# Kernel tuning notes

Hardware: AMD Instinct MI355X
Metric: run time of the kernel (lower is better)

The kernel has to match this reference:

```python
import jax, jax.numpy as jnp
import numpy as np

NH = 16
D = 1024
B, T = 4, 4096


def setup_inputs() -> dict:
    key = jax.random.key(0)
    k1, k2, k3, k4 = jax.random.split(key, 4)
    x = jax.random.normal(k1, (B, T, D), dtype=jnp.float32)
    phi = jax.random.normal(k2, (B, T), dtype=jnp.float32)
    W_attn = jax.random.normal(k3, (D, D), dtype=jnp.float32) * 0.02
    W_proj = jax.random.normal(k4, (D, D), dtype=jnp.float32) * 0.02
    gamma = jnp.ones((NH, 1), dtype=jnp.float32)
    temp = jnp.ones((NH, 1), dtype=jnp.float32)
    return {"x": x, "phi": phi, "W_attn": W_attn, "W_proj": W_proj,
            "gamma": gamma, "temp": temp}


def reference(x, phi, W_attn, W_proj, gamma, temp):
    Bb, Tt, d = x.shape
    hd = d // NH
    # c_attn (no bias), split heads: [B, nh, T, hd]
    w = (x @ W_attn.T).reshape(Bb, Tt, NH, hd).transpose(0, 2, 1, 3)
    w_sq = w * w
    denom = jnp.maximum(jnp.cumsum(w_sq, axis=-2), 1e-12)
    w_norm = w_sq / denom
    tssa_score = w_norm.sum(-1) * temp                       # [B, nh, T]
    phi_Q = phi[:, None, :]                                  # [B, 1, T]
    steps = jnp.arange(1, Tt + 1, dtype=x.dtype)
    mean_phi = jnp.cumsum(phi, axis=-1)[:, None, :] / steps  # running mean of phi
    penalty = (phi_Q - mean_phi) ** 2                        # [B, 1, T]
    score = tssa_score - gamma * penalty                     # [B, nh, T]
    alpha = jax.nn.softmax(score, axis=1)                    # softmax over HEADS (dim=1)
    dots = jnp.cumsum(w_sq * alpha[..., None], axis=-2) / (
        jnp.cumsum(alpha, axis=-1)[..., None] + 1e-8)
    attn = jnp.minimum(1.0 / (1.0 + dots), 10000.0)
    y = -w * alpha[..., None] * attn                          # [B, nh, T, hd]
    y = y.transpose(0, 2, 1, 3).reshape(Bb, Tt, d)
    y = y @ W_proj.T                                          # dropout is identity (p=0 / eval)
    return (y, alpha)
```

## Files before the change

### kernel.cpp

```cpp
#include <hip/hip_runtime.h>
#include <hip/hip_bf16.h>
#include <stdint.h>

#define NHh 16
#define Dm  1024
#define HD  64
#define Bb  4
#define Tt  4096
#define NCH 128
#define CHL 32

#define BM 256
#define BN 256
#define BK 64
#define NKT (Dm / BK)

using bf16 = __hip_bfloat16;
typedef __attribute__((ext_vector_type(8))) short short8;
typedef __attribute__((ext_vector_type(4))) float f32x4;

__device__ __forceinline__ float bf2f(bf16 v) { return __bfloat162float(v); }

__device__ __forceinline__ float b2f(unsigned short u) {
  union { unsigned int i; float f; } x; x.i = ((unsigned int)u) << 16; return x.f;
}

__device__ __forceinline__ float frcp(float x) {
  float r; asm("v_rcp_f32 %0, %1" : "=v"(r) : "v"(x)); return r;
}

__device__ __forceinline__ void gld_lds16(const void* g, void* l) {
  __builtin_amdgcn_global_load_lds(
      (const __attribute__((address_space(1))) unsigned int*)g,
      (__attribute__((address_space(3))) unsigned int*)l, 16, 0, 0);
}

template <bool OUT_BF16, bool WRITE_S1>
__global__ __launch_bounds__(512, 2) void gemm256(const bf16* __restrict__ A,
                                                  const bf16* __restrict__ W,
                                                  void* __restrict__ Cout,
                                                  float* __restrict__ S1,
                                                  int M, int N, int K) {
  extern __shared__ char smem[];
  const int tid  = threadIdx.x;
  const int lane = tid & 63;
  const int wave = tid >> 6;
  const int bid = blockIdx.x;
  const int swz = (bid & 7) * 32 + (bid >> 3);
  const int bn = (swz & 3) * BN;
  const int bm = (swz >> 2) * BM;
  const int wm = (wave >> 1) * 64;
  const int wn = (wave & 1) * 128;
  const int quad = lane >> 4;
  const int l16  = lane & 15;

  const int srow = wave * 8 + (lane >> 3);
  const int scol = (((lane & 7) ^ (lane >> 3)) << 3);

  const bf16* Abase = A + (size_t)(bm + srow) * K + scol;
  const bf16* Wbase = W + (size_t)(bn + srow) * K + scol;

  f32x4 acc[4][8] = {};

#define SLAB_A(buf, n) (smem + (buf) * 65536 + (n) * 8192 + wave * 1024)
#define SLAB_B(buf, n) (smem + (buf) * 65536 + 32768 + (n) * 8192 + wave * 1024)
#define STAGE_A(buf, n, k0) gld_lds16(Abase + (size_t)(n) * 64 * K + (k0), SLAB_A(buf, n))
#define STAGE_B(buf, n, k0) gld_lds16(Wbase + (size_t)(n) * 64 * K + (k0), SLAB_B(buf, n))
#define LD_FRAG(base, r, s) (*(const short8*)((base) + (size_t)(r) * 128 + ((((s) ^ ((r) & 7))) << 4)))

  STAGE_A(0, 0, 0); STAGE_A(0, 1, 0); STAGE_A(0, 2, 0); STAGE_A(0, 3, 0);
  STAGE_B(0, 0, 0); STAGE_B(0, 1, 0); STAGE_B(0, 2, 0); STAGE_B(0, 3, 0);
  asm volatile("s_waitcnt vmcnt(0)" ::: "memory");
  __builtin_amdgcn_s_barrier();
  __builtin_amdgcn_sched_barrier(0);

  short8 af[4][2], bfv[4][2];
  for (int t = 0; t < NKT; t++) {
    const int buf = t & 1;
    const char* aL = smem + buf * 65536;
    const char* bL = aL + 32768;
    const int k0n = (t + 1) * BK;
    const bool pf = (t + 1 < NKT);

    if (pf) {
      STAGE_A(buf ^ 1, 0, k0n); STAGE_A(buf ^ 1, 1, k0n);
      STAGE_A(buf ^ 1, 2, k0n); STAGE_A(buf ^ 1, 3, k0n);
      STAGE_B(buf ^ 1, 0, k0n); STAGE_B(buf ^ 1, 2, k0n);
    }
#pragma unroll
    for (int mi = 0; mi < 4; mi++) {
      const int r = wm + mi * 16 + l16;
      af[mi][0] = LD_FRAG(aL, r, quad);
      af[mi][1] = LD_FRAG(aL, r, quad + 4);
    }
#pragma unroll
    for (int nj = 0; nj < 4; nj++) {
      const int r = wn + nj * 16 + l16;
      bfv[nj][0] = LD_FRAG(bL, r, quad);
      bfv[nj][1] = LD_FRAG(bL, r, quad + 4);
    }
    __builtin_amdgcn_s_setprio(1);
#pragma unroll
    for (int mi = 0; mi < 4; mi++)
#pragma unroll
      for (int nj = 0; nj < 4; nj++) {
        acc[mi][nj] = __builtin_amdgcn_mfma_f32_16x16x32_bf16(af[mi][0], bfv[nj][0], acc[mi][nj], 0, 0, 0);
        acc[mi][nj] = __builtin_amdgcn_mfma_f32_16x16x32_bf16(af[mi][1], bfv[nj][1], acc[mi][nj], 0, 0, 0);
      }
    __builtin_amdgcn_s_setprio(0);
    if (pf) { asm volatile("s_waitcnt vmcnt(6)" ::: "memory"); }
    else    { asm volatile("s_waitcnt vmcnt(0)" ::: "memory"); }
    __builtin_amdgcn_s_barrier();
    __builtin_amdgcn_sched_barrier(0);

    if (pf) { STAGE_B(buf ^ 1, 1, k0n); STAGE_B(buf ^ 1, 3, k0n); }
#pragma unroll
    for (int nj = 0; nj < 4; nj++) {
      const int r = wn + 64 + nj * 16 + l16;
      bfv[nj][0] = LD_FRAG(bL, r, quad);
      bfv[nj][1] = LD_FRAG(bL, r, quad + 4);
    }
    __builtin_amdgcn_s_setprio(1);
#pragma unroll
    for (int mi = 0; mi < 4; mi++)
#pragma unroll
      for (int nj = 0; nj < 4; nj++) {
        acc[mi][nj + 4] = __builtin_amdgcn_mfma_f32_16x16x32_bf16(af[mi][0], bfv[nj][0], acc[mi][nj + 4], 0, 0, 0);
        acc[mi][nj + 4] = __builtin_amdgcn_mfma_f32_16x16x32_bf16(af[mi][1], bfv[nj][1], acc[mi][nj + 4], 0, 0, 0);
      }
    __builtin_amdgcn_s_setprio(0);
    asm volatile("s_waitcnt vmcnt(2)" ::: "memory");
    __builtin_amdgcn_s_barrier();
    __builtin_amdgcn_sched_barrier(0);
  }

#pragma unroll
  for (int nj = 0; nj < 8; nj++) {
    const int col = bn + wn + nj * 16 + l16;
    if constexpr (OUT_BF16) {
      float ss0 = 0.f, ss1 = 0.f;
#pragma unroll
      for (int mi = 0; mi < 4; mi++) {
        float csum = 0.f;
#pragma unroll
        for (int r = 0; r < 4; r++) {
          const int row = bm + wm + mi * 16 + quad * 4 + r;
          const bf16 hv = __float2bfloat16(acc[mi][nj][r]);
          ((bf16*)Cout)[(size_t)row * N + col] = hv;
          if constexpr (WRITE_S1) { const float fv = bf2f(hv); csum += fv * fv; }
        }
        if constexpr (WRITE_S1) { if (mi < 2) ss0 += csum; else ss1 += csum; }
      }
      if constexpr (WRITE_S1) {
        ss0 += __shfl_xor(ss0, 16, 64); ss0 += __shfl_xor(ss0, 32, 64);
        ss1 += __shfl_xor(ss1, 16, 64); ss1 += __shfl_xor(ss1, 32, 64);
        if (quad == 0) {
          const int h = col >> 6, d = col & 63;
          const int r0 = bm + wm;
          const int b  = r0 >> 12;
          const int c0 = (r0 & (Tt - 1)) >> 5;
          float* s1p = S1 + (((size_t)(b * NHh + h) * NCH) + c0) * HD + d;
          s1p[0]  = ss0;
          s1p[HD] = ss1;
        }
      }
    } else {
#pragma unroll
      for (int mi = 0; mi < 4; mi++)
#pragma unroll
        for (int r = 0; r < 4; r++) {
          const int row = bm + wm + mi * 16 + quad * 4 + r;
          ((float*)Cout)[(size_t)row * N + col] = acc[mi][nj][r];
        }
    }
  }
#undef SLAB_A
#undef SLAB_B
#undef STAGE_A
#undef STAGE_B
#undef LD_FRAG
}

__global__ __launch_bounds__(256) void prep(const float* __restrict__ x,
                                            const float* __restrict__ Wa,
                                            const float* __restrict__ Wp,
                                            const float* __restrict__ phi,
                                            bf16* __restrict__ x_bf,
                                            bf16* __restrict__ Wa_bf,
                                            bf16* __restrict__ Wp_bf,
                                            float* __restrict__ penalty) {
  const int bid = blockIdx.x;
  if (bid < 1536) {
    const float* in;
    bf16* out;
    int n, nblk, b0;
    if (bid < 1024)      { in = x;  out = x_bf;  n = Bb * Tt * Dm; nblk = 1024; b0 = 0; }
    else if (bid < 1280) { in = Wa; out = Wa_bf; n = Dm * Dm;      nblk = 256;  b0 = 1024; }
    else                 { in = Wp; out = Wp_bf; n = Dm * Dm;      nblk = 256;  b0 = 1280; }
    const int stride = nblk * 256;
    for (int i = (bid - b0) * 256 + threadIdx.x; i * 4 < n; i += stride) {
      const float4 v = *(const float4*)(in + (size_t)i * 4);
      ushort4 o;
      o.x = __bfloat16_as_ushort(__float2bfloat16(v.x));
      o.y = __bfloat16_as_ushort(__float2bfloat16(v.y));
      o.z = __bfloat16_as_ushort(__float2bfloat16(v.z));
      o.w = __bfloat16_as_ushort(__float2bfloat16(v.w));
      *(ushort4*)(out + (size_t)i * 4) = o;
    }
  } else {
    const int b = bid - 1536;
    const int tid = threadIdx.x;
    const int lane = tid & 63, wid = tid >> 6;
    __shared__ float wsum[4];
    __shared__ float carry_s;
    if (tid == 0) carry_s = 0.f;
    __syncthreads();
    for (int r = 0; r < Tt / 256; r++) {
      const int t = r * 256 + tid;
      const float v = phi[b * Tt + t];
      float incl = v;
#pragma unroll
      for (int off = 1; off < 64; off <<= 1) {
        float nn = __shfl_up(incl, off, 64);
        if (lane >= off) incl += nn;
      }
      if (lane == 63) wsum[wid] = incl;
      __syncthreads();
      float woff = carry_s;
      for (int wpre = 0; wpre < wid; wpre++) woff += wsum[wpre];
      const float csum = woff + incl;
      const float mean = csum / (float)(t + 1);
      const float dphi = v - mean;
      penalty[b * Tt + t] = dphi * dphi;
      __syncthreads();
      if (tid == 0) carry_s += wsum[0] + wsum[1] + wsum[2] + wsum[3];
      __syncthreads();
    }
  }
}

__global__ __launch_bounds__(256) void mid_fused(const bf16* __restrict__ w,
                                                 const float* __restrict__ S1,
                                                 const float* __restrict__ temp,
                                                 const float* __restrict__ gamma,
                                                 const float* __restrict__ penalty,
                                                 float* __restrict__ alpha_f,
                                                 float* __restrict__ S2,
                                                 float* __restrict__ SA) {
  const int c = blockIdx.x, b = blockIdx.y;
  const int tid = threadIdx.x, h = tid >> 4, l = tid & 15;
  __shared__ float sm_t[CHL][NHh + 1];
  __shared__ float sm_a[CHL][NHh + 1];
  __shared__ float sm_g[NHh], sm_tv[NHh];
  if (tid < NHh) { sm_g[tid] = gamma[tid]; sm_tv[tid] = temp[tid]; }

  const float4* p4 = (const float4*)(S1 + (((size_t)(b * NHh + h) * NCH)) * HD + l * 4);
  float4 s0 = {0,0,0,0}, s1v = {0,0,0,0}, s2v = {0,0,0,0}, s3v = {0,0,0,0};
  int cc = 0;
  for (; cc + 4 <= c; cc += 4) {
    const float4 v0 = p4[(size_t)cc * 16];
    const float4 v1 = p4[(size_t)(cc + 1) * 16];
    const float4 v2 = p4[(size_t)(cc + 2) * 16];
    const float4 v3 = p4[(size_t)(cc + 3) * 16];
    s0.x += v0.x; s0.y += v0.y; s0.z += v0.z; s0.w += v0.w;
    s1v.x += v1.x; s1v.y += v1.y; s1v.z += v1.z; s1v.w += v1.w;
    s2v.x += v2.x; s2v.y += v2.y; s2v.z += v2.z; s2v.w += v2.w;
    s3v.x += v3.x; s3v.y += v3.y; s3v.z += v3.z; s3v.w += v3.w;
  }
  for (; cc < c; cc++) {
    const float4 v0 = p4[(size_t)cc * 16];
    s0.x += v0.x; s0.y += v0.y; s0.z += v0.z; s0.w += v0.w;
  }
  float a0 = s0.x + s1v.x + s2v.x + s3v.x;
  float a1 = s0.y + s1v.y + s2v.y + s3v.y;
  float a2 = s0.z + s1v.z + s2v.z + s3v.z;
  float a3 = s0.w + s1v.w + s2v.w + s3v.w;
  __syncthreads();

  const bf16* wp = w + ((size_t)(b * Tt + c * CHL)) * Dm + h * HD + l * 4;
  const float tv = sm_tv[h];
#pragma unroll 8
  for (int i = 0; i < CHL; i++) {
    const ushort4 v = *(const ushort4*)(wp + (size_t)i * Dm);
    const float f0 = b2f(v.x), f1 = b2f(v.y), f2 = b2f(v.z), f3 = b2f(v.w);
    const float q0 = f0 * f0, q1 = f1 * f1, q2 = f2 * f2, q3 = f3 * f3;
    a0 += q0; a1 += q1; a2 += q2; a3 += q3;
    float val = q0 * frcp(fmaxf(a0, 1e-12f)) + q1 * frcp(fmaxf(a1, 1e-12f))
              + q2 * frcp(fmaxf(a2, 1e-12f)) + q3 * frcp(fmaxf(a3, 1e-12f));
    val += __shfl_xor(val, 1, 64);
    val += __shfl_xor(val, 2, 64);
    val += __shfl_xor(val, 4, 64);
    val += __shfl_xor(val, 8, 64);
    if (l == 0) sm_t[i][h] = tv * val;
  }
  __syncthreads();

  if (tid < CHL) {
    const int t = tid;
    const float pen = penalty[(size_t)b * Tt + c * CHL + t];
    float sc[NHh];
    float mx = -1e30f;
#pragma unroll
    for (int hh = 0; hh < NHh; hh++) {
      sc[hh] = sm_t[t][hh] - sm_g[hh] * pen;
      mx = fmaxf(mx, sc[hh]);
    }
    float sum = 0.f;
#pragma unroll
    for (int hh = 0; hh < NHh; hh++) { const float e = __expf(sc[hh] - mx); sc[hh] = e; sum += e; }
    const float inv = 1.f / sum;
#pragma unroll
    for (int hh = 0; hh < NHh; hh++) sm_a[t][hh] = sc[hh] * inv;
  }
  __syncthreads();

#pragma unroll
  for (int k2 = 0; k2 < CHL / 16; k2++) {
    const int t = k2 * 16 + l;
    alpha_f[((size_t)(b * NHh + h)) * Tt + c * CHL + t] = sm_a[t][h];
  }

  float d0 = 0.f, d1 = 0.f, d2 = 0.f, d3 = 0.f, sa = 0.f;
#pragma unroll 8
  for (int i = 0; i < CHL; i++) {
    const float a = sm_a[i][h];
    const ushort4 v = *(const ushort4*)(wp + (size_t)i * Dm);
    const float f0 = b2f(v.x), f1 = b2f(v.y), f2 = b2f(v.z), f3 = b2f(v.w);
    d0 += f0 * f0 * a; d1 += f1 * f1 * a; d2 += f2 * f2 * a; d3 += f3 * f3 * a;
    sa += a;
  }
  float4 o; o.x = d0; o.y = d1; o.z = d2; o.w = d3;
  *(float4*)&S2[(((size_t)(b * NHh + h) * NCH) + c) * HD + l * 4] = o;
  if (l == 0) SA[(size_t)(b * NHh + h) * NCH + c] = sa;
}

__global__ __launch_bounds__(256) void y_phase3(const bf16* __restrict__ w,
                                                const float* __restrict__ alpha_f,
                                                const float* __restrict__ S2,
                                                const float* __restrict__ SA,
                                                bf16* __restrict__ yprime) {
  const int c = blockIdx.x, b = blockIdx.y;
  const int tid = threadIdx.x, h = tid >> 4, l = tid & 15;

  const float* sap = SA + (size_t)(b * NHh + h) * NCH;
  float sa_part = 0.f;
  for (int cc = l; cc < c; cc += 16) sa_part += sap[cc];
  sa_part += __shfl_xor(sa_part, 1, 64);
  sa_part += __shfl_xor(sa_part, 2, 64);
  sa_part += __shfl_xor(sa_part, 4, 64);
  sa_part += __shfl_xor(sa_part, 8, 64);
  float acca = sa_part;

  const float4* p4 = (const float4*)(S2 + (((size_t)(b * NHh + h) * NCH)) * HD + l * 4);
  float4 s0 = {0,0,0,0}, s1v = {0,0,0,0}, s2v = {0,0,0,0}, s3v = {0,0,0,0};
  int cc = 0;
  for (; cc + 4 <= c; cc += 4) {
    const float4 v0 = p4[(size_t)cc * 16];
    const float4 v1 = p4[(size_t)(cc + 1) * 16];
    const float4 v2 = p4[(size_t)(cc + 2) * 16];
    const float4 v3 = p4[(size_t)(cc + 3) * 16];
    s0.x += v0.x; s0.y += v0.y; s0.z += v0.z; s0.w += v0.w;
    s1v.x += v1.x; s1v.y += v1.y; s1v.z += v1.z; s1v.w += v1.w;
    s2v.x += v2.x; s2v.y += v2.y; s2v.z += v2.z; s2v.w += v2.w;
    s3v.x += v3.x; s3v.y += v3.y; s3v.z += v3.z; s3v.w += v3.w;
  }
  for (; cc < c; cc++) {
    const float4 v0 = p4[(size_t)cc * 16];
    s0.x += v0.x; s0.y += v0.y; s0.z += v0.z; s0.w += v0.w;
  }
  float a0 = s0.x + s1v.x + s2v.x + s3v.x;
  float a1 = s0.y + s1v.y + s2v.y + s3v.y;
  float a2 = s0.z + s1v.z + s2v.z + s3v.z;
  float a3 = s0.w + s1v.w + s2v.w + s3v.w;

  const bf16* wp = w + ((size_t)(b * Tt + c * CHL)) * Dm + h * HD + l * 4;
  const float* ap = alpha_f + (size_t)(b * NHh + h) * Tt + c * CHL;
  bf16* yp = yprime + ((size_t)(b * Tt + c * CHL)) * Dm + h * HD + l * 4;
#pragma unroll 8
  for (int i = 0; i < CHL; i++) {
    const float a = ap[i];
    const ushort4 v = *(const ushort4*)(wp + (size_t)i * Dm);
    const float f0 = b2f(v.x), f1 = b2f(v.y), f2 = b2f(v.z), f3 = b2f(v.w);
    a0 += f0 * f0 * a; a1 += f1 * f1 * a; a2 += f2 * f2 * a; a3 += f3 * f3 * a;
    acca += a;
    const float rinv = frcp(acca + 1e-8f);
    const float at0 = fminf(frcp(1.f + a0 * rinv), 10000.f);
    const float at1 = fminf(frcp(1.f + a1 * rinv), 10000.f);
    const float at2 = fminf(frcp(1.f + a2 * rinv), 10000.f);
    const float at3 = fminf(frcp(1.f + a3 * rinv), 10000.f);
    ushort4 o;
    o.x = __bfloat16_as_ushort(__float2bfloat16(-f0 * a * at0));
    o.y = __bfloat16_as_ushort(__float2bfloat16(-f1 * a * at1));
    o.z = __bfloat16_as_ushort(__float2bfloat16(-f2 * a * at2));
    o.w = __bfloat16_as_ushort(__float2bfloat16(-f3 * a * at3));
    *(ushort4*)(yp + (size_t)i * Dm) = o;
  }
}

extern "C" void kernel_launch(void* const* d_in, const int* in_sizes, int n_in,
                              void* d_out, int out_size, void* d_ws, size_t ws_size,
                              hipStream_t stream) {
  const float* x     = (const float*)d_in[0];
  const float* phi   = (const float*)d_in[1];
  const float* Wattn = (const float*)d_in[2];
  const float* Wproj = (const float*)d_in[3];
  const float* gamma = (const float*)d_in[4];
  const float* temp  = (const float*)d_in[5];

  float* y_out    = (float*)d_out;
  float* alpha_f  = y_out + (size_t)Bb * Tt * Dm;

  char* ws = (char*)d_ws;
  bf16*  x_bf   = (bf16*)ws;  ws += (size_t)Bb * Tt * Dm * 2;
  bf16*  Wa_bf  = (bf16*)ws;  ws += (size_t)Dm * Dm * 2;
  bf16*  Wp_bf  = (bf16*)ws;  ws += (size_t)Dm * Dm * 2;
  bf16*  w_bf   = (bf16*)ws;  ws += (size_t)Bb * Tt * Dm * 2;
  float* pen    = (float*)ws; ws += (size_t)Bb * Tt * 4;
  float* S1     = (float*)ws; ws += (size_t)Bb * NHh * NCH * HD * 4;
  float* S2     = (float*)ws; ws += (size_t)Bb * NHh * NCH * HD * 4;
  float* SA     = (float*)ws; ws += (size_t)Bb * NHh * NCH * 4;
  bf16*  yprime = x_bf;

  static int attr_done = 0;
  if (!attr_done) {
    hipFuncSetAttribute((const void*)gemm256<true, true>,
                        hipFuncAttributeMaxDynamicSharedMemorySize, 131072);
    hipFuncSetAttribute((const void*)gemm256<false, false>,
                        hipFuncAttributeMaxDynamicSharedMemorySize, 131072);
    attr_done = 1;
  }

  const int M = Bb * Tt, N = Dm, K = Dm;
  dim3 gg((M / BM) * (N / BN)), gb(512);

  prep<<<dim3(1540), dim3(256), 0, stream>>>(x, Wattn, Wproj, phi, x_bf, Wa_bf, Wp_bf, pen);
  gemm256<true, true><<<gg, gb, 131072, stream>>>(x_bf, Wa_bf, (void*)w_bf, S1, M, N, K);
  mid_fused<<<dim3(NCH, Bb), dim3(256), 0, stream>>>(w_bf, S1, temp, gamma, pen,
                                                     alpha_f, S2, SA);
  y_phase3<<<dim3(NCH, Bb), dim3(256), 0, stream>>>(w_bf, alpha_f, S2, SA, yprime);
  gemm256<false, false><<<gg, gb, 131072, stream>>>(yprime, Wp_bf, (void*)y_out, nullptr, M, N, K);
}
```

Measured before the change: 253.7 us.

## Fuse fp32-to-bf16 conversion of x into first GEMM and stage bf16 output via LDS

The first GEMM now reads x directly as fp32, converts it to bf16 in registers and writes the swizzled tile into LDS. This removes the separate prep pass that wrote and re-read a bf16 copy of x. The bf16 output tile is also staged through LDS so it can be written to global memory in coalesced 16-byte chunks instead of scattered 2-byte stores. In exchange the A loads become register-routed with more vmcnt bookkeeping, use more VGPRs and fetch twice the bytes per k-tile.

```diff
diff --git a/kernel.cpp b/kernel.cpp
--- a/kernel.cpp
+++ b/kernel.cpp
@@ -35,8 +35,21 @@
       (__attribute__((address_space(3))) unsigned int*)l, 16, 0, 0);
 }
 
-template <bool OUT_BF16, bool WRITE_S1>
-__global__ __launch_bounds__(512, 2) void gemm256(const bf16* __restrict__ A,
+__device__ __forceinline__ short8 pack8(const float4& a, const float4& b) {
+  short8 r;
+  r[0] = (short)__bfloat16_as_ushort(__float2bfloat16(a.x));
+  r[1] = (short)__bfloat16_as_ushort(__float2bfloat16(a.y));
+  r[2] = (short)__bfloat16_as_ushort(__float2bfloat16(a.z));
+  r[3] = (short)__bfloat16_as_ushort(__float2bfloat16(a.w));
+  r[4] = (short)__bfloat16_as_ushort(__float2bfloat16(b.x));
+  r[5] = (short)__bfloat16_as_ushort(__float2bfloat16(b.y));
+  r[6] = (short)__bfloat16_as_ushort(__float2bfloat16(b.z));
+  r[7] = (short)__bfloat16_as_ushort(__float2bfloat16(b.w));
+  return r;
+}
+
+template <bool A_FP32, bool OUT_BF16, bool WRITE_S1>
+__global__ __launch_bounds__(512, 2) void gemm256(const void* __restrict__ Ain,
                                                   const bf16* __restrict__ W,
                                                   void* __restrict__ Cout,
                                                   float* __restrict__ S1,
@@ -57,47 +70,66 @@
   const int srow = wave * 8 + (lane >> 3);
   const int scol = (((lane & 7) ^ (lane >> 3)) << 3);
 
-  const bf16* Abase = A + (size_t)(bm + srow) * K + scol;
-  const bf16* Wbase = W + (size_t)(bn + srow) * K + scol;
+  const bf16*  Abase  = A_FP32 ? nullptr : ((const bf16*)Ain + (size_t)(bm + srow) * K + scol);
+  const float* Afbase = A_FP32 ? ((const float*)Ain + (size_t)(bm + srow) * K + scol) : nullptr;
+  const bf16*  Wbase  = W + (size_t)(bn + srow) * K + scol;
 
   f32x4 acc[4][8] = {};
+  float4 aL[4][2];
 
 #define SLAB_A(buf, n) (smem + (buf) * 65536 + (n) * 8192 + wave * 1024)
 #define SLAB_B(buf, n) (smem + (buf) * 65536 + 32768 + (n) * 8192 + wave * 1024)
 #define STAGE_A(buf, n, k0) gld_lds16(Abase + (size_t)(n) * 64 * K + (k0), SLAB_A(buf, n))
 #define STAGE_B(buf, n, k0) gld_lds16(Wbase + (size_t)(n) * 64 * K + (k0), SLAB_B(buf, n))
+#define LOADA(n, k0) do {                                                    \
+    const float* p_ = Afbase + (size_t)(n) * 64 * K + (k0);                  \
+    aL[n][0] = *(const float4*)p_;                                           \
+    aL[n][1] = *(const float4*)(p_ + 4);                                     \
+  } while (0)
+#define WRITEA(buf, n) do {                                                  \
+    *(short8*)(SLAB_A(buf, n) + lane * 16) = pack8(aL[n][0], aL[n][1]);      \
+  } while (0)
 #define LD_FRAG(base, r, s) (*(const short8*)((base) + (size_t)(r) * 128 + ((((s) ^ ((r) & 7))) << 4)))
 
-  STAGE_A(0, 0, 0); STAGE_A(0, 1, 0); STAGE_A(0, 2, 0); STAGE_A(0, 3, 0);
-  STAGE_B(0, 0, 0); STAGE_B(0, 1, 0); STAGE_B(0, 2, 0); STAGE_B(0, 3, 0);
-  asm volatile("s_waitcnt vmcnt(0)" ::: "memory");
+  if constexpr (A_FP32) {
+    LOADA(0, 0); LOADA(1, 0); LOADA(2, 0); LOADA(3, 0);
+    STAGE_B(0, 0, 0); STAGE_B(0, 1, 0); STAGE_B(0, 2, 0); STAGE_B(0, 3, 0);
+    asm volatile("s_waitcnt vmcnt(4)" ::: "memory");
+    WRITEA(0, 0); WRITEA(0, 1); WRITEA(0, 2); WRITEA(0, 3);
+    asm volatile("s_waitcnt vmcnt(0) lgkmcnt(0)" ::: "memory");
+  } else {
+    STAGE_A(0, 0, 0); STAGE_A(0, 1, 0); STAGE_A(0, 2, 0); STAGE_A(0, 3, 0);
+    STAGE_B(0, 0, 0); STAGE_B(0, 1, 0); STAGE_B(0, 2, 0); STAGE_B(0, 3, 0);
+    asm volatile("s_waitcnt vmcnt(0)" ::: "memory");
+  }
   __builtin_amdgcn_s_barrier();
   __builtin_amdgcn_sched_barrier(0);
 
   short8 af[4][2], bfv[4][2];
   for (int t = 0; t < NKT; t++) {
     const int buf = t & 1;
-    const char* aL = smem + buf * 65536;
-    const char* bL = aL + 32768;
+    const char* aLd = smem + buf * 65536;
+    const char* bLd = aLd + 32768;
     const int k0n = (t + 1) * BK;
     const bool pf = (t + 1 < NKT);
 
     if (pf) {
-      STAGE_A(buf ^ 1, 0, k0n); STAGE_A(buf ^ 1, 1, k0n);
-      STAGE_A(buf ^ 1, 2, k0n); STAGE_A(buf ^ 1, 3, k0n);
+      if constexpr (A_FP32) { LOADA(0, k0n); LOADA(1, k0n); LOADA(2, k0n); LOADA(3, k0n); }
+      else { STAGE_A(buf ^ 1, 0, k0n); STAGE_A(buf ^ 1, 1, k0n);
+             STAGE_A(buf ^ 1, 2, k0n); STAGE_A(buf ^ 1, 3, k0n); }
       STAGE_B(buf ^ 1, 0, k0n); STAGE_B(buf ^ 1, 2, k0n);
     }
 #pragma unroll
     for (int mi = 0; mi < 4; mi++) {
       const int r = wm + mi * 16 + l16;
-      af[mi][0] = LD_FRAG(aL, r, quad);
-      af[mi][1] = LD_FRAG(aL, r, quad + 4);
+      af[mi][0] = LD_FRAG(aLd, r, quad);
+      af[mi][1] = LD_FRAG(aLd, r, quad + 4);
     }
 #pragma unroll
     for (int nj = 0; nj < 4; nj++) {
       const int r = wn + nj * 16 + l16;
-      bfv[nj][0] = LD_FRAG(bL, r, quad);
-      bfv[nj][1] = LD_FRAG(bL, r, quad + 4);
+      bfv[nj][0] = LD_FRAG(bLd, r, quad);
+      bfv[nj][1] = LD_FRAG(bLd, r, quad + 4);
     }
     __builtin_amdgcn_s_setprio(1);
 #pragma unroll
@@ -108,18 +140,26 @@
         acc[mi][nj] = __builtin_amdgcn_mfma_f32_16x16x32_bf16(af[mi][1], bfv[nj][1], acc[mi][nj], 0, 0, 0);
       }
     __builtin_amdgcn_s_setprio(0);
-    if (pf) { asm volatile("s_waitcnt vmcnt(6)" ::: "memory"); }
-    else    { asm volatile("s_waitcnt vmcnt(0)" ::: "memory"); }
+    if (pf) {
+      if constexpr (A_FP32) { asm volatile("s_waitcnt vmcnt(10)" ::: "memory"); }
+      else                  { asm volatile("s_waitcnt vmcnt(6)" ::: "memory"); }
+    } else { asm volatile("s_waitcnt vmcnt(0)" ::: "memory"); }
     __builtin_amdgcn_s_barrier();
     __builtin_amdgcn_sched_barrier(0);
 
-    if (pf) { STAGE_B(buf ^ 1, 1, k0n); STAGE_B(buf ^ 1, 3, k0n); }
+    if (pf) {
+      if constexpr (A_FP32) {
+        asm volatile("s_waitcnt vmcnt(2)" ::: "memory");
+        WRITEA(buf ^ 1, 0); WRITEA(buf ^ 1, 1); WRITEA(buf ^ 1, 2); WRITEA(buf ^ 1, 3);
+      }
+    }
 #pragma unroll
     for (int nj = 0; nj < 4; nj++) {
       const int r = wn + 64 + nj * 16 + l16;
-      bfv[nj][0] = LD_FRAG(bL, r, quad);
-      bfv[nj][1] = LD_FRAG(bL, r, quad + 4);
-    }
+      bfv[nj][0] = LD_FRAG(bLd, r, quad);
+      bfv[nj][1] = LD_FRAG(bLd, r, quad + 4);
+    }
+    if (pf) { STAGE_B(buf ^ 1, 1, k0n); STAGE_B(buf ^ 1, 3, k0n); }
     __builtin_amdgcn_s_setprio(1);
 #pragma unroll
     for (int mi = 0; mi < 4; mi++)
@@ -129,24 +169,27 @@
         acc[mi][nj + 4] = __builtin_amdgcn_mfma_f32_16x16x32_bf16(af[mi][1], bfv[nj][1], acc[mi][nj + 4], 0, 0, 0);
       }
     __builtin_amdgcn_s_setprio(0);
-    asm volatile("s_waitcnt vmcnt(2)" ::: "memory");
+    if (pf) { asm volatile("s_waitcnt vmcnt(2) lgkmcnt(0)" ::: "memory"); }
+    else    { asm volatile("s_waitcnt vmcnt(0) lgkmcnt(0)" ::: "memory"); }
     __builtin_amdgcn_s_barrier();
     __builtin_amdgcn_sched_barrier(0);
   }
 
-#pragma unroll
-  for (int nj = 0; nj < 8; nj++) {
-    const int col = bn + wn + nj * 16 + l16;
-    if constexpr (OUT_BF16) {
+  if constexpr (OUT_BF16) {
+    ushort* cst = (ushort*)smem;
+#pragma unroll
+    for (int nj = 0; nj < 8; nj++) {
+      const int gcol = bn + wn + nj * 16 + l16;
       float ss0 = 0.f, ss1 = 0.f;
 #pragma unroll
       for (int mi = 0; mi < 4; mi++) {
         float csum = 0.f;
 #pragma unroll
         for (int r = 0; r < 4; r++) {
-          const int row = bm + wm + mi * 16 + quad * 4 + r;
+          const int row = wm + mi * 16 + quad * 4 + r;
+          const int col = wn + nj * 16 + l16;
           const bf16 hv = __float2bfloat16(acc[mi][nj][r]);
-          ((bf16*)Cout)[(size_t)row * N + col] = hv;
+          cst[(row * 512 + ((col * 2) ^ ((row & 7) << 4))) >> 1] = __bfloat16_as_ushort(hv);
           if constexpr (WRITE_S1) { const float fv = bf2f(hv); csum += fv * fv; }
         }
         if constexpr (WRITE_S1) { if (mi < 2) ss0 += csum; else ss1 += csum; }
@@ -155,7 +198,7 @@
         ss0 += __shfl_xor(ss0, 16, 64); ss0 += __shfl_xor(ss0, 32, 64);
         ss1 += __shfl_xor(ss1, 16, 64); ss1 += __shfl_xor(ss1, 32, 64);
         if (quad == 0) {
-          const int h = col >> 6, d = col & 63;
+          const int h = gcol >> 6, d = gcol & 63;
           const int r0 = bm + wm;
           const int b  = r0 >> 12;
           const int c0 = (r0 & (Tt - 1)) >> 5;
@@ -164,7 +207,21 @@
           s1p[HD] = ss1;
         }
       }
-    } else {
+    }
+    asm volatile("s_waitcnt lgkmcnt(0)" ::: "memory");
+    __builtin_amdgcn_s_barrier();
+#pragma unroll
+    for (int it = 0; it < 16; it++) {
+      const int idx = it * 512 + tid;
+      const int row = idx >> 5;
+      const int ch  = idx & 31;
+      const short8 v = *(const short8*)(smem + row * 512 + ((ch ^ (row & 7)) << 4));
+      *(short8*)((bf16*)Cout + (size_t)(bm + row) * N + bn + ch * 8) = v;
+    }
+  } else {
+#pragma unroll
+    for (int nj = 0; nj < 8; nj++) {
+      const int col = bn + wn + nj * 16 + l16;
 #pragma unroll
       for (int mi = 0; mi < 4; mi++)
 #pragma unroll
@@ -178,26 +235,24 @@
 #undef SLAB_B
 #undef STAGE_A
 #undef STAGE_B
+#undef LOADA
+#undef WRITEA
 #undef LD_FRAG
 }
 
-__global__ __launch_bounds__(256) void prep(const float* __restrict__ x,
-                                            const float* __restrict__ Wa,
+__global__ __launch_bounds__(256) void prep(const float* __restrict__ Wa,
                                             const float* __restrict__ Wp,
                                             const float* __restrict__ phi,
-                                            bf16* __restrict__ x_bf,
                                             bf16* __restrict__ Wa_bf,
                                             bf16* __restrict__ Wp_bf,
                                             float* __restrict__ penalty) {
   const int bid = blockIdx.x;
-  if (bid < 1536) {
-    const float* in;
-    bf16* out;
-    int n, nblk, b0;
-    if (bid < 1024)      { in = x;  out = x_bf;  n = Bb * Tt * Dm; nblk = 1024; b0 = 0; }
-    else if (bid < 1280) { in = Wa; out = Wa_bf; n = Dm * Dm;      nblk = 256;  b0 = 1024; }
-    else                 { in = Wp; out = Wp_bf; n = Dm * Dm;      nblk = 256;  b0 = 1280; }
-    const int stride = nblk * 256;
+  if (bid < 512) {
+    const float* in = (bid < 256) ? Wa : Wp;
+    bf16* out = (bid < 256) ? Wa_bf : Wp_bf;
+    const int b0 = (bid < 256) ? 0 : 256;
+    const int n = Dm * Dm;
+    const int stride = 256 * 256;
     for (int i = (bid - b0) * 256 + threadIdx.x; i * 4 < n; i += stride) {
       const float4 v = *(const float4*)(in + (size_t)i * 4);
       ushort4 o;
@@ -208,7 +263,7 @@
       *(ushort4*)(out + (size_t)i * 4) = o;
     }
   } else {
-    const int b = bid - 1536;
+    const int b = bid - 512;
     const int tid = threadIdx.x;
     const int lane = tid & 63, wid = tid >> 6;
     __shared__ float wsum[4];
@@ -411,21 +466,20 @@
   float* alpha_f  = y_out + (size_t)Bb * Tt * Dm;
 
   char* ws = (char*)d_ws;
-  bf16*  x_bf   = (bf16*)ws;  ws += (size_t)Bb * Tt * Dm * 2;
   bf16*  Wa_bf  = (bf16*)ws;  ws += (size_t)Dm * Dm * 2;
   bf16*  Wp_bf  = (bf16*)ws;  ws += (size_t)Dm * Dm * 2;
   bf16*  w_bf   = (bf16*)ws;  ws += (size_t)Bb * Tt * Dm * 2;
+  bf16*  yprime = (bf16*)ws;  ws += (size_t)Bb * Tt * Dm * 2;
   float* pen    = (float*)ws; ws += (size_t)Bb * Tt * 4;
   float* S1     = (float*)ws; ws += (size_t)Bb * NHh * NCH * HD * 4;
   float* S2     = (float*)ws; ws += (size_t)Bb * NHh * NCH * HD * 4;
   float* SA     = (float*)ws; ws += (size_t)Bb * NHh * NCH * 4;
-  bf16*  yprime = x_bf;
 
   static int attr_done = 0;
   if (!attr_done) {
-    hipFuncSetAttribute((const void*)gemm256<true, true>,
+    hipFuncSetAttribute((const void*)gemm256<true, true, true>,
                         hipFuncAttributeMaxDynamicSharedMemorySize, 131072);
-    hipFuncSetAttribute((const void*)gemm256<false, false>,
+    hipFuncSetAttribute((const void*)gemm256<false, false, false>,
                         hipFuncAttributeMaxDynamicSharedMemorySize, 131072);
     attr_done = 1;
   }
@@ -433,10 +487,10 @@
   const int M = Bb * Tt, N = Dm, K = Dm;
   dim3 gg((M / BM) * (N / BN)), gb(512);
 
-  prep<<<dim3(1540), dim3(256), 0, stream>>>(x, Wattn, Wproj, phi, x_bf, Wa_bf, Wp_bf, pen);
-  gemm256<true, true><<<gg, gb, 131072, stream>>>(x_bf, Wa_bf, (void*)w_bf, S1, M, N, K);
+  prep<<<dim3(516), dim3(256), 0, stream>>>(Wattn, Wproj, phi, Wa_bf, Wp_bf, pen);
+  gemm256<true, true, true><<<gg, gb, 131072, stream>>>(x, Wa_bf, (void*)w_bf, S1, M, N, K);
   mid_fused<<<dim3(NCH, Bb), dim3(256), 0, stream>>>(w_bf, S1, temp, gamma, pen,
                                                      alpha_f, S2, SA);
   y_phase3<<<dim3(NCH, Bb), dim3(256), 0, stream>>>(w_bf, alpha_f, S2, SA, yprime);
-  gemm256<false, false><<<gg, gb, 131072, stream>>>(yprime, Wp_bf, (void*)y_out, nullptr, M, N, K);
-}
+  gemm256<false, false, false><<<gg, gb, 131072, stream>>>(yprime, Wp_bf, (void*)y_out, nullptr, M, N, K);
+}
```

Result: slower. 270.1 us (+6.5%).

## Shrink GEMM tiles to 256x128x32 with simpler double-buffered pipeline

Applied to the files above, without the earlier changes.

Changes the bf16 GEMM from 256x256x64 tiles to 256x128x32 tiles, which cuts LDS use per block from 128KB to 48KB and raises the launch-bounds occupancy hint from 2 to 4. The staggered B-slab prefetch with partial vmcnt waits is replaced by one full-wait barrier per k-step, and the block swizzle is adjusted for 8 column tiles. The aim is more blocks in flight and better CU coverage (512 blocks instead of 256), at the cost of less data reuse per tile, twice as many barriers and no overlap of loads inside a k-step.

```diff
diff --git a/kernel.cpp b/kernel.cpp
--- a/kernel.cpp
+++ b/kernel.cpp
@@ -11,8 +11,8 @@
 #define CHL 32
 
 #define BM 256
-#define BN 256
-#define BK 64
+#define BN 128
+#define BK 32
 #define NKT (Dm / BK)
 
 using bf16 = __hip_bfloat16;
@@ -36,7 +36,7 @@
 }
 
 template <bool OUT_BF16, bool WRITE_S1>
-__global__ __launch_bounds__(512, 2) void gemm256(const bf16* __restrict__ A,
+__global__ __launch_bounds__(512, 4) void gemm256(const bf16* __restrict__ A,
                                                   const bf16* __restrict__ W,
                                                   void* __restrict__ Cout,
                                                   float* __restrict__ S1,
@@ -46,96 +46,60 @@
   const int lane = tid & 63;
   const int wave = tid >> 6;
   const int bid = blockIdx.x;
-  const int swz = (bid & 7) * 32 + (bid >> 3);
-  const int bn = (swz & 3) * BN;
-  const int bm = (swz >> 2) * BM;
+  const int swz = (bid & 7) * 64 + (bid >> 3);
+  const int bn = (swz & 7) * BN;
+  const int bm = (swz >> 3) * BM;
   const int wm = (wave >> 1) * 64;
-  const int wn = (wave & 1) * 128;
+  const int wn = (wave & 1) * 64;
   const int quad = lane >> 4;
   const int l16  = lane & 15;
 
-  const int srow = wave * 8 + (lane >> 3);
-  const int scol = (((lane & 7) ^ (lane >> 3)) << 3);
+  const int srow = wave * 16 + (lane >> 2);
+  const int scol = (((lane & 3) ^ ((lane >> 3) & 3)) << 3);
 
   const bf16* Abase = A + (size_t)(bm + srow) * K + scol;
   const bf16* Wbase = W + (size_t)(bn + srow) * K + scol;
 
-  f32x4 acc[4][8] = {};
-
-#define SLAB_A(buf, n) (smem + (buf) * 65536 + (n) * 8192 + wave * 1024)
-#define SLAB_B(buf, n) (smem + (buf) * 65536 + 32768 + (n) * 8192 + wave * 1024)
-#define STAGE_A(buf, n, k0) gld_lds16(Abase + (size_t)(n) * 64 * K + (k0), SLAB_A(buf, n))
-#define STAGE_B(buf, n, k0) gld_lds16(Wbase + (size_t)(n) * 64 * K + (k0), SLAB_B(buf, n))
-#define LD_FRAG(base, r, s) (*(const short8*)((base) + (size_t)(r) * 128 + ((((s) ^ ((r) & 7))) << 4)))
-
-  STAGE_A(0, 0, 0); STAGE_A(0, 1, 0); STAGE_A(0, 2, 0); STAGE_A(0, 3, 0);
-  STAGE_B(0, 0, 0); STAGE_B(0, 1, 0); STAGE_B(0, 2, 0); STAGE_B(0, 3, 0);
+  f32x4 acc[4][4] = {};
+
+#define SLAB_A(buf, n) (smem + (buf) * 24576 + (n) * 8192 + wave * 1024)
+#define SLAB_B(buf)    (smem + (buf) * 24576 + 16384 + wave * 1024)
+#define STAGE_A(buf, n, k0) gld_lds16(Abase + (size_t)(n) * 128 * K + (k0), SLAB_A(buf, n))
+#define STAGE_B(buf, k0)    gld_lds16(Wbase + (k0), SLAB_B(buf))
+#define LD_FRAG(sb, r, c) (*(const short8*)((sb) + (size_t)(r) * 64 + ((((c) ^ (((r) >> 1) & 3))) << 4)))
+
+  STAGE_A(0, 0, 0); STAGE_A(0, 1, 0); STAGE_B(0, 0);
   asm volatile("s_waitcnt vmcnt(0)" ::: "memory");
   __builtin_amdgcn_s_barrier();
   __builtin_amdgcn_sched_barrier(0);
 
-  short8 af[4][2], bfv[4][2];
+  short8 af[4], bf8[4];
   for (int t = 0; t < NKT; t++) {
     const int buf = t & 1;
-    const char* aL = smem + buf * 65536;
-    const char* bL = aL + 32768;
+    const char* aL = smem + buf * 24576;
+    const char* bL = aL + 16384;
     const int k0n = (t + 1) * BK;
-    const bool pf = (t + 1 < NKT);
-
-    if (pf) {
-      STAGE_A(buf ^ 1, 0, k0n); STAGE_A(buf ^ 1, 1, k0n);
-      STAGE_A(buf ^ 1, 2, k0n); STAGE_A(buf ^ 1, 3, k0n);
-      STAGE_B(buf ^ 1, 0, k0n); STAGE_B(buf ^ 1, 2, k0n);
+    if (t + 1 < NKT) {
+      STAGE_A(buf ^ 1, 0, k0n); STAGE_A(buf ^ 1, 1, k0n); STAGE_B(buf ^ 1, k0n);
     }
 #pragma unroll
-    for (int mi = 0; mi < 4; mi++) {
-      const int r = wm + mi * 16 + l16;
-      af[mi][0] = LD_FRAG(aL, r, quad);
-      af[mi][1] = LD_FRAG(aL, r, quad + 4);
-    }
-#pragma unroll
-    for (int nj = 0; nj < 4; nj++) {
-      const int r = wn + nj * 16 + l16;
-      bfv[nj][0] = LD_FRAG(bL, r, quad);
-      bfv[nj][1] = LD_FRAG(bL, r, quad + 4);
-    }
+    for (int mi = 0; mi < 4; mi++) af[mi]  = LD_FRAG(aL, wm + mi * 16 + l16, quad);
+#pragma unroll
+    for (int nj = 0; nj < 4; nj++) bf8[nj] = LD_FRAG(bL, wn + nj * 16 + l16, quad);
     __builtin_amdgcn_s_setprio(1);
 #pragma unroll
     for (int mi = 0; mi < 4; mi++)
 #pragma unroll
-      for (int nj = 0; nj < 4; nj++) {
-        acc[mi][nj] = __builtin_amdgcn_mfma_f32_16x16x32_bf16(af[mi][0], bfv[nj][0], acc[mi][nj], 0, 0, 0);
-        acc[mi][nj] = __builtin_amdgcn_mfma_f32_16x16x32_bf16(af[mi][1], bfv[nj][1], acc[mi][nj], 0, 0, 0);
-      }
+      for (int nj = 0; nj < 4; nj++)
+        acc[mi][nj] = __builtin_amdgcn_mfma_f32_16x16x32_bf16(af[mi], bf8[nj], acc[mi][nj], 0, 0, 0);
     __builtin_amdgcn_s_setprio(0);
-    if (pf) { asm volatile("s_waitcnt vmcnt(6)" ::: "memory"); }
-    else    { asm volatile("s_waitcnt vmcnt(0)" ::: "memory"); }
+    asm volatile("s_waitcnt vmcnt(0)" ::: "memory");
     __builtin_amdgcn_s_barrier();
     __builtin_amdgcn_sched_barrier(0);
-
-    if (pf) { STAGE_B(buf ^ 1, 1, k0n); STAGE_B(buf ^ 1, 3, k0n); }
-#pragma unroll
-    for (int nj = 0; nj < 4; nj++) {
-      const int r = wn + 64 + nj * 16 + l16;
-      bfv[nj][0] = LD_FRAG(bL, r, quad);
-      bfv[nj][1] = LD_FRAG(bL, r, quad + 4);
-    }
-    __builtin_amdgcn_s_setprio(1);
-#pragma unroll
-    for (int mi = 0; mi < 4; mi++)
-#pragma unroll
-      for (int nj = 0; nj < 4; nj++) {
-        acc[mi][nj + 4] = __builtin_amdgcn_mfma_f32_16x16x32_bf16(af[mi][0], bfv[nj][0], acc[mi][nj + 4], 0, 0, 0);
-        acc[mi][nj + 4] = __builtin_amdgcn_mfma_f32_16x16x32_bf16(af[mi][1], bfv[nj][1], acc[mi][nj + 4], 0, 0, 0);
-      }
-    __builtin_amdgcn_s_setprio(0);
-    asm volatile("s_waitcnt vmcnt(2)" ::: "memory");
-    __builtin_amdgcn_s_barrier();
-    __builtin_amdgcn_sched_barrier(0);
-  }
-
-#pragma unroll
-  for (int nj = 0; nj < 8; nj++) {
+  }
+
+#pragma unroll
+  for (int nj = 0; nj < 4; nj++) {
     const int col = bn + wn + nj * 16 + l16;
     if constexpr (OUT_BF16) {
       float ss0 = 0.f, ss1 = 0.f;
@@ -424,9 +388,9 @@
   static int attr_done = 0;
   if (!attr_done) {
     hipFuncSetAttribute((const void*)gemm256<true, true>,
-                        hipFuncAttributeMaxDynamicSharedMemorySize, 131072);
+                        hipFuncAttributeMaxDynamicSharedMemorySize, 49152);
     hipFuncSetAttribute((const void*)gemm256<false, false>,
-                        hipFuncAttributeMaxDynamicSharedMemorySize, 131072);
+                        hipFuncAttributeMaxDynamicSharedMemorySize, 49152);
     attr_done = 1;
   }
 
@@ -434,9 +398,9 @@
   dim3 gg((M / BM) * (N / BN)), gb(512);
 
   prep<<<dim3(1540), dim3(256), 0, stream>>>(x, Wattn, Wproj, phi, x_bf, Wa_bf, Wp_bf, pen);
-  gemm256<true, true><<<gg, gb, 131072, stream>>>(x_bf, Wa_bf, (void*)w_bf, S1, M, N, K);
+  gemm256<true, true><<<gg, gb, 49152, stream>>>(x_bf, Wa_bf, (void*)w_bf, S1, M, N, K);
   mid_fused<<<dim3(NCH, Bb), dim3(256), 0, stream>>>(w_bf, S1, temp, gamma, pen,
                                                      alpha_f, S2, SA);
   y_phase3<<<dim3(NCH, Bb), dim3(256), 0, stream>>>(w_bf, alpha_f, S2, SA, yprime);
-  gemm256<false, false><<<gg, gb, 131072, stream>>>(yprime, Wp_bf, (void*)y_out, nullptr, M, N, K);
-}
+  gemm256<false, false><<<gg, gb, 49152, stream>>>(yprime, Wp_bf, (void*)y_out, nullptr, M, N, K);
+}
```

Measured after the change: 265.1 us. +4.5%, slower.
